# Optimization experiments

Measured on AMD Instinct MI355X. Metric: run time of the kernel, lower is better.

## Reference

```python
import jax, jax.numpy as jnp
import numpy as np

EMBED = 1024
HEADS = 16
HEAD_DIM = EMBED // HEADS
MLP = 4 * EMBED
EPS = 1e-6


def setup_inputs() -> dict:
    key = jax.random.key(0)
    ks = jax.random.split(key, 16)
    B, N, C = 2, 2048, EMBED
    x = jax.random.normal(ks[0], (B, N, C), dtype=jnp.float32)
    c = jax.random.normal(ks[1], (B, C), dtype=jnp.float32)
    attention_mask = jax.random.randint(ks[2], (B, N), 0, 2, dtype=jnp.int32)
    s = 0.02
    params = {
        "norm_w": jnp.ones((C,), jnp.float32),
        "scale_w": s * jax.random.normal(ks[3], (C, C), jnp.float32),
        "scale_b": s * jax.random.normal(ks[4], (C,), jnp.float32),
        "shift_w": s * jax.random.normal(ks[5], (C, C), jnp.float32),
        "shift_b": s * jax.random.normal(ks[6], (C,), jnp.float32),
        "qkv_w": s * jax.random.normal(ks[7], (3 * C, C), jnp.float32),
        "proj_w": s * jax.random.normal(ks[8], (C, C), jnp.float32),
        "proj_b": s * jax.random.normal(ks[9], (C,), jnp.float32),
        "mlp_w1": s * jax.random.normal(ks[10], (2 * MLP, C), jnp.float32),
        "mlp_b1": s * jax.random.normal(ks[11], (2 * MLP,), jnp.float32),
        "mlp_w2": s * jax.random.normal(ks[12], (C, MLP), jnp.float32),
        "mlp_b2": s * jax.random.normal(ks[13], (C,), jnp.float32),
    }
    return {"x": x, "c": c, "attention_mask": attention_mask, **params}


def _adaln(x, c, norm_w, scale_w, scale_b, shift_w, shift_b):
    sc = jax.nn.silu(c)
    shift = sc @ shift_w.T + shift_b                      # [B,C]
    scale = jnp.clip(sc @ scale_w.T + scale_b + 1.0, 0.1, 10.0)
    # RMSNorm: ||x|| * C^-0.5, clamped below by eps
    norm = jnp.maximum(jnp.linalg.norm(x, axis=-1, keepdims=True) * x.shape[-1] ** -0.5, EPS)
    h = x / norm * norm_w
    return h * scale[:, None, :] + shift[:, None, :]


def _attention(x, attention_mask, qkv_w, proj_w, proj_b):
    B, N, C = x.shape
    qkv = (x @ qkv_w.T).reshape(B, N, 3, HEADS, HEAD_DIM)
    q = qkv[:, :, 0].transpose(0, 2, 1, 3)  # [B,H,N,D]
    k = qkv[:, :, 1].transpose(0, 2, 1, 3)
    v = qkv[:, :, 2].transpose(0, 2, 1, 3)
    attn = jnp.einsum("bhnd,bhmd->bhnm", q, k) * (HEAD_DIM ** -0.5)
    mask = attention_mask[:, None, None, :]              # [B,1,1,N] over keys
    attn = jnp.where(mask == 0, -jnp.inf, attn)
    all_inf = jnp.all(attn == -jnp.inf, axis=-1, keepdims=True)
    attn = jnp.where(all_inf, 0.0, attn)
    p = jax.nn.softmax(attn, axis=-1)
    out = jnp.einsum("bhnm,bhmd->bhnd", p, v).transpose(0, 2, 1, 3).reshape(B, N, C)
    return out @ proj_w.T + proj_b


def _mlp(x, w1, b1, w2, b2):
    h = x @ w1.T + b1
    x1, x2 = jnp.split(h, 2, axis=-1)
    return (jax.nn.silu(x1) * x2) @ w2.T + b2


def reference(x, c, attention_mask, norm_w, scale_w, scale_b, shift_w, shift_b,
              qkv_w, proj_w, proj_b, mlp_w1, mlp_b1, mlp_w2, mlp_b2):
    x = x + _attention(_adaln(x, c, norm_w, scale_w, scale_b, shift_w, shift_b),
                       attention_mask, qkv_w, proj_w, proj_b)
    x = x + _mlp(_adaln(x, c, norm_w, scale_w, scale_b, shift_w, shift_b),
                 mlp_w1, mlp_b1, mlp_w2, mlp_b2)
    return x
```

## Files before the change

### kernel.cpp

```cpp
#include <hip/hip_runtime.h>
#include <cstdint>
#include <cstddef>

#define DEVINL __device__ __forceinline__

typedef __bf16 bf16x8 __attribute__((ext_vector_type(8)));
typedef float  f32x4  __attribute__((ext_vector_type(4)));


DEVINL unsigned short f2b(float f) {
  unsigned u = __builtin_bit_cast(unsigned, f);
  u += 0x7fffu + ((u >> 16) & 1u);
  return (unsigned short)(u >> 16);
}

DEVINL unsigned packtrunc(float a, float b) {
  unsigned ua = __builtin_bit_cast(unsigned, a);
  unsigned ub = __builtin_bit_cast(unsigned, b);
  return (ua >> 16) | (ub & 0xffff0000u);
}

DEVINL void async16(void* lds, const void* g) {
  __builtin_amdgcn_global_load_lds((const __attribute__((address_space(1))) unsigned*)g,
                                   (__attribute__((address_space(3))) unsigned*)lds,
                                   16, 0, 0);
}


__global__ void cvt4_kernel(const float* __restrict__ s0, const float* __restrict__ s1,
                            const float* __restrict__ s2, const float* __restrict__ s3,
                            unsigned short* __restrict__ d0, unsigned short* __restrict__ d1,
                            unsigned short* __restrict__ d2, unsigned short* __restrict__ d3) {
  int i = blockIdx.x * 256 + threadIdx.x;
  if (i < 786432) {
    float4 v = ((const float4*)s0)[i];
    ushort4 o; o.x = f2b(v.x); o.y = f2b(v.y); o.z = f2b(v.z); o.w = f2b(v.w);
    ((ushort4*)d0)[i] = o;
  } else if (i < 1048576) {
    int off = i - 786432;
    float4 v = ((const float4*)s1)[off];
    ushort4 o; o.x = f2b(v.x); o.y = f2b(v.y); o.z = f2b(v.z); o.w = f2b(v.w);
    ((ushort4*)d1)[off] = o;
  } else if (i < 3145728) {
    int off = i - 1048576;
    int row = off >> 8, col = off & 255;
    int rp = (row < 4096) ? (row << 1) : (((row - 4096) << 1) | 1);
    float4 v = ((const float4*)s2)[off];
    ushort4 o; o.x = f2b(v.x); o.y = f2b(v.y); o.z = f2b(v.z); o.w = f2b(v.w);
    ((ushort4*)d2)[rp * 256 + col] = o;
  } else {
    int off = i - 3145728;
    float4 v = ((const float4*)s3)[off];
    ushort4 o; o.x = f2b(v.x); o.y = f2b(v.y); o.z = f2b(v.z); o.w = f2b(v.w);
    ((ushort4*)d3)[off] = o;
  }
}


__global__ void cond_kernel(const float* __restrict__ c,
                            const float* __restrict__ scale_w, const float* __restrict__ scale_b,
                            const float* __restrict__ shift_w, const float* __restrict__ shift_b,
                            float* __restrict__ scale_o, float* __restrict__ shift_o) {
  __shared__ float sc[1024];
  __shared__ float red[2][4][64];
  int tid = threadIdx.x;
  int b = blockIdx.x >> 4, ch = blockIdx.x & 15;
  for (int i = tid; i < 1024; i += 256) {
    float cv = c[b * 1024 + i];
    sc[i] = cv / (1.f + __expf(-cv));
  }
  __syncthreads();
  int colidx = tid & 63, p = tid >> 6;
  int co = ch * 64 + colidx;
  float dsc = 0.f, dsh = 0.f;
  for (int i = 0; i < 256; ++i) {
    int kk = p * 256 + i;
    float s = sc[kk];
    dsc += s * scale_w[(size_t)co * 1024 + kk];
    dsh += s * shift_w[(size_t)co * 1024 + kk];
  }
  red[0][p][colidx] = dsc;
  red[1][p][colidx] = dsh;
  __syncthreads();
  if (p == 0) {
    float s4  = red[0][0][colidx] + red[0][1][colidx] + red[0][2][colidx] + red[0][3][colidx];
    float sh4 = red[1][0][colidx] + red[1][1][colidx] + red[1][2][colidx] + red[1][3][colidx];
    scale_o[b * 1024 + co] = fminf(fmaxf(s4 + scale_b[co] + 1.f, 0.1f), 10.f);
    shift_o[b * 1024 + co] = sh4 + shift_b[co];
  }
}


__global__ __launch_bounds__(256) void adaln_kernel(const float* __restrict__ x,
                                                    const float* __restrict__ norm_w,
                                                    const float* __restrict__ scale,
                                                    const float* __restrict__ shift,
                                                    unsigned short* __restrict__ h) {
  int row = blockIdx.x;
  int b = row >> 11;
  int tid = threadIdx.x;
  float4 v = ((const float4*)(x + (size_t)row * 1024))[tid];
  float ss = v.x * v.x + v.y * v.y + v.z * v.z + v.w * v.w;
  #pragma unroll
  for (int d = 32; d; d >>= 1) ss += __shfl_xor(ss, d);
  __shared__ float wsum[4];
  if ((tid & 63) == 0) wsum[tid >> 6] = ss;
  __syncthreads();
  float tot = wsum[0] + wsum[1] + wsum[2] + wsum[3];
  float inv = 1.f / fmaxf(sqrtf(tot * (1.f / 1024.f)), 1e-6f);
  float4 nw  = ((const float4*)norm_w)[tid];
  float4 scv = ((const float4*)(scale + b * 1024))[tid];
  float4 shv = ((const float4*)(shift + b * 1024))[tid];
  ushort4 o;
  o.x = f2b(v.x * inv * nw.x * scv.x + shv.x);
  o.y = f2b(v.y * inv * nw.y * scv.y + shv.y);
  o.z = f2b(v.z * inv * nw.z * scv.z + shv.z);
  o.w = f2b(v.w * inv * nw.w * scv.w + shv.w);
  ((ushort4*)(h + (size_t)row * 1024))[tid] = o;
}


template<int EPI, int MT>
__global__ __launch_bounds__(256, 1) void gemm_k(
    const unsigned short* __restrict__ A,
    const unsigned short* __restrict__ B0,
    const float* __restrict__ bias0,
    const float* __restrict__ resid,
    void* __restrict__ out0_, void* __restrict__ out1_, void* __restrict__ out2_,
    int M, int N, int K) {
  constexpr int MI = MT / 32;
  constexpr int A_SH = MT * 32;
  constexpr int COMPUTE_SH = 2 * A_SH + 2 * 4096;
  constexpr int STAGE_SH = (EPI == 1) ? 128 * 136 : (EPI == 2 ? 128 * 72 : 0);
  constexpr int SMEM_SH = (COMPUTE_SH > STAGE_SH) ? COMPUTE_SH : STAGE_SH;
  __shared__ __align__(16) unsigned short smem[SMEM_SH];
  unsigned short* As0 = smem;
  unsigned short* As1 = smem + A_SH;
  unsigned short* Bs0 = smem + 2 * A_SH;
  unsigned short* Bs1 = smem + 2 * A_SH + 4096;

  const int tid = threadIdx.x;
  const int wave = tid >> 6, lane = tid & 63;
  const int quad = lane >> 4, l16 = lane & 15;
  const int wm = (wave >> 1) * (MT / 2), wn = (wave & 1) * 64;
  const int bm = blockIdx.y * MT, bn = blockIdx.x * 128;

  f32x4 acc[MI][4] = {};

  const int steps = K >> 6;
  for (int s = 0; s < steps; ++s) {
    const int k0 = s << 6;
    __syncthreads();
    #pragma unroll
    for (int i = 0; i < MT / 64; ++i) {
      int cc = i * 256 + tid;
      int r = cc >> 2, ko = (cc & 3) << 3;
      size_t ga = (size_t)(bm + r) * K + k0 + ko;
      async16(As0 + (i * 2048 + wave * 512), A + ga);
      async16(As1 + (i * 2048 + wave * 512), A + ga + 32);
    }
    #pragma unroll
    for (int i = 0; i < 2; ++i) {
      int cc = i * 256 + tid;
      int r = cc >> 2, ko = (cc & 3) << 3;
      size_t gb = (size_t)(bn + r) * K + k0 + ko;
      async16(Bs0 + (i * 2048 + wave * 512), B0 + gb);
      async16(Bs1 + (i * 2048 + wave * 512), B0 + gb + 32);
    }
    __syncthreads();
    #pragma unroll
    for (int ks = 0; ks < 2; ++ks) {
      const unsigned short* Ah = ks ? As1 : As0;
      const unsigned short* Bh = ks ? Bs1 : Bs0;
      bf16x8 af[MI], bfr[4];
      #pragma unroll
      for (int mi = 0; mi < MI; ++mi)
        af[mi] = *reinterpret_cast<const bf16x8*>(&Ah[(wm + mi * 16 + l16) * 32 + quad * 8]);
      #pragma unroll
      for (int ni = 0; ni < 4; ++ni)
        bfr[ni] = *reinterpret_cast<const bf16x8*>(&Bh[(wn + ni * 16 + l16) * 32 + quad * 8]);
      #pragma unroll
      for (int mi = 0; mi < MI; ++mi)
        #pragma unroll
        for (int ni = 0; ni < 4; ++ni)
          acc[mi][ni] = __builtin_amdgcn_mfma_f32_16x16x32_bf16(af[mi], bfr[ni], acc[mi][ni], 0, 0, 0);
    }
  }

  if constexpr (EPI == 0) {
    #pragma unroll
    for (int mi = 0; mi < MI; ++mi) {
      #pragma unroll
      for (int ni = 0; ni < 4; ++ni) {
        int gc = bn + wn + ni * 16 + l16;
        #pragma unroll
        for (int r = 0; r < 4; ++r) {
          int gr = bm + wm + mi * 16 + quad * 4 + r;
          ((float*)out0_)[(size_t)gr * N + gc] = acc[mi][ni][r] + bias0[gc] + resid[(size_t)gr * N + gc];
        }
      }
    }
  } else if constexpr (EPI == 1) {
    const int region = bn >> 10;
    __syncthreads();
    #pragma unroll
    for (int mi = 0; mi < MI; ++mi) {
      #pragma unroll
      for (int ni = 0; ni < 4; ++ni) {
        int lc = wn + ni * 16 + l16;
        #pragma unroll
        for (int r = 0; r < 4; ++r) {
          int lr = wm + mi * 16 + quad * 4 + r;
          float v = acc[mi][ni][r];
          if (region == 0)      smem[lr * 136 + lc] = f2b(v * 0.125f);
          else if (region == 1) smem[lr * 136 + lc] = f2b(v);
          else                  smem[lc * 136 + lr] = f2b(v);
        }
      }
    }
    __syncthreads();
    const int b = bm >> 11;
    const int bnm = bn & 1023;
    if (region <= 1) {
      int lr = tid >> 1, hl = tid & 1;
      int n = (bm + lr) & 2047;
      int hh = (bnm >> 6) + hl;
      unsigned short* dst = (unsigned short*)(region == 0 ? out0_ : out1_) +
                            (((size_t)(b * 16 + hh)) * 2048 + n) * 64;
      const unsigned short* src = smem + lr * 136 + hl * 64;
      #pragma unroll
      for (int j = 0; j < 8; ++j)
        ((uint4*)dst)[j] = *(const uint4*)(src + j * 8);
    } else {
      int lc = tid >> 1, nh = tid & 1;
      int c2 = bnm + lc;
      int hh = c2 >> 6, d = c2 & 63;
      int nbase = (bm & 2047) + nh * 64;
      unsigned short* dst = (unsigned short*)out2_ +
                            (((size_t)(b * 16 + hh)) * 64 + d) * 2048 + nbase;
      const unsigned short* src = smem + lc * 136 + nh * 64;
      #pragma unroll
      for (int j = 0; j < 8; ++j)
        ((uint4*)dst)[j] = *(const uint4*)(src + j * 8);
    }
  } else {
    __syncthreads();
    #pragma unroll
    for (int mi = 0; mi < MI; ++mi) {
      #pragma unroll
      for (int ni = 0; ni < 4; ++ni) {
        int lc = wn + ni * 16 + l16;
        int gcp = bn + lc;
        int gi = gcp >> 1;
        float bias = bias0[(gcp & 1) ? 4096 + gi : gi];
        #pragma unroll
        for (int r = 0; r < 4; ++r) {
          int lr = wm + mi * 16 + quad * 4 + r;
          float v = acc[mi][ni][r] + bias;
          float p = __shfl_xor(v, 1);
          if ((l16 & 1) == 0) {
            float g = (v / (1.f + __expf(-v))) * p;
            smem[lr * 72 + (lc >> 1)] = f2b(g);
          }
        }
      }
    }
    __syncthreads();
    int lr = tid >> 1, ch = (tid & 1) * 32;
    unsigned short* dst = (unsigned short*)out0_ + (size_t)(bm + lr) * (N >> 1) + (bn >> 1) + ch;
    const unsigned short* src = smem + lr * 72 + ch;
    #pragma unroll
    for (int j = 0; j < 4; ++j)
      ((uint4*)dst)[j] = *(const uint4*)(src + j * 8);
  }
}


__global__ __launch_bounds__(512, 2) void gemm256_glu(
    const unsigned short* __restrict__ A,
    const unsigned short* __restrict__ B,
    const float* __restrict__ bias,
    unsigned short* __restrict__ out,
    int M, int N, int K) {
  __shared__ __align__(16) unsigned short smem[65536];

  const int tid  = threadIdx.x;
  const int wave = tid >> 6, lane = tid & 63;
  const int quad = lane >> 4, l16 = lane & 15;
  const int wm = (wave >> 2) * 128, wn = (wave & 3) * 64;

  const int lin = blockIdx.y * gridDim.x + blockIdx.x;
  const int xcd = lin & 7, idx = lin >> 3;
  const int bx = (xcd << 2) + (idx & 3);
  const int by = idx >> 2;
  const int bm = by * 256, bn = bx * 256;

  const int srow = tid >> 3;
  const int slc  = (tid & 7) ^ (srow & 7);
  const unsigned short* gA0 = A + (size_t)(bm + srow) * K + slc * 8;
  const unsigned short* gB0 = B + (size_t)(bn + srow) * K + slc * 8;
  const size_t rstep = (size_t)64 * K;

#define STAGE_A(h, tk, d) do { \
    const unsigned short* s_ = gA0 + (size_t)(h) * 128 * K + (size_t)(tk) * 64; \
    async16(smem + (d) * 16384 + (h) * 8192 + tid * 8, s_); \
    async16(smem + (d) * 16384 + (h) * 8192 + 4096 + tid * 8, s_ + rstep); \
  } while (0)
#define STAGE_B(h, tk, d) do { \
    const unsigned short* s_ = gB0 + (size_t)(h) * 128 * K + (size_t)(tk) * 64; \
    async16(smem + 32768 + (d) * 16384 + (h) * 8192 + tid * 8, s_); \
    async16(smem + 32768 + (d) * 16384 + (h) * 8192 + 4096 + tid * 8, s_ + rstep); \
  } while (0)

  const int pc0 = (quad ^ (l16 & 7)) * 8;
  const int pc1 = ((quad + 4) ^ (l16 & 7)) * 8;
  const int arow = wm + l16;
  const int brow = wn + l16;

  f32x4 acc[8][4] = {};
  bf16x8 bfr[4][2];
  const int T = K >> 6;
  const int JI = T >> 1;

  STAGE_B(0, 0, 0); STAGE_B(1, 0, 0);
  STAGE_A(0, 0, 0); STAGE_A(1, 0, 0);
  STAGE_B(0, 1, 1); STAGE_B(1, 1, 1);
  asm volatile("s_waitcnt vmcnt(4)" ::: "memory");
  __builtin_amdgcn_s_barrier();

#define READ_BFR(d) do { \
    _Pragma("unroll") \
    for (int ni = 0; ni < 4; ++ni) { \
      int rb = 32768 + (d) * 16384 + (brow + ni * 16) * 64; \
      bfr[ni][0] = *reinterpret_cast<const bf16x8*>(&smem[rb + pc0]); \
      bfr[ni][1] = *reinterpret_cast<const bf16x8*>(&smem[rb + pc1]); \
    } \
  } while (0)

#define PHASE(d, q, RB, STAGE_STMT, TAIL_STMT) do { \
    bf16x8 a00, a01, a10, a11; \
    if (RB) READ_BFR(d); \
    { int ra = (d) * 16384 + (arow + (2 * (q)) * 16) * 64; \
      a00 = *reinterpret_cast<const bf16x8*>(&smem[ra + pc0]); \
      a01 = *reinterpret_cast<const bf16x8*>(&smem[ra + pc1]); \
      a10 = *reinterpret_cast<const bf16x8*>(&smem[ra + 1024 + pc0]); \
      a11 = *reinterpret_cast<const bf16x8*>(&smem[ra + 1024 + pc1]); } \
    STAGE_STMT; \
    if (RB) asm volatile("s_waitcnt lgkmcnt(8)" ::: "memory"); \
    __builtin_amdgcn_s_barrier(); \
    asm volatile("s_waitcnt lgkmcnt(0)" ::: "memory"); \
    __builtin_amdgcn_sched_barrier(0); \
    __builtin_amdgcn_s_setprio(1); \
    _Pragma("unroll") \
    for (int ni = 0; ni < 4; ++ni) \
      acc[2 * (q)][ni] = __builtin_amdgcn_mfma_f32_16x16x32_bf16(a00, bfr[ni][0], acc[2 * (q)][ni], 0, 0, 0); \
    _Pragma("unroll") \
    for (int ni = 0; ni < 4; ++ni) \
      acc[2 * (q) + 1][ni] = __builtin_amdgcn_mfma_f32_16x16x32_bf16(a10, bfr[ni][0], acc[2 * (q) + 1][ni], 0, 0, 0); \
    _Pragma("unroll") \
    for (int ni = 0; ni < 4; ++ni) \
      acc[2 * (q)][ni] = __builtin_amdgcn_mfma_f32_16x16x32_bf16(a01, bfr[ni][1], acc[2 * (q)][ni], 0, 0, 0); \
    _Pragma("unroll") \
    for (int ni = 0; ni < 4; ++ni) \
      acc[2 * (q) + 1][ni] = __builtin_amdgcn_mfma_f32_16x16x32_bf16(a11, bfr[ni][1], acc[2 * (q) + 1][ni], 0, 0, 0); \
    __builtin_amdgcn_s_setprio(0); \
    TAIL_STMT; \
    __builtin_amdgcn_s_barrier(); \
  } while (0)

  for (int j = 0; j < JI; ++j) {
    const int t1 = 2 * j + 1, t2 = 2 * j + 2, t3 = 2 * j + 3;
    const bool g2 = (t2 < T), g3 = (t3 < T);
    PHASE(0, 0, 1, { STAGE_A(0, t1, 1); }, {});
    PHASE(0, 1, 0, { STAGE_A(1, t1, 1); }, {});
    PHASE(0, 2, 0, { if (g2) STAGE_B(0, t2, 0); }, {});
    PHASE(0, 3, 0, { if (g2) STAGE_B(1, t2, 0); },
          { if (g2) { asm volatile("s_waitcnt vmcnt(4)" ::: "memory"); }
            else    { asm volatile("s_waitcnt vmcnt(0)" ::: "memory"); } });
    PHASE(1, 0, 1, { if (g2) STAGE_A(0, t2, 0); }, {});
    PHASE(1, 1, 0, { if (g2) STAGE_A(1, t2, 0); }, {});
    PHASE(1, 2, 0, { if (g3) STAGE_B(0, t3, 1); }, {});
    PHASE(1, 3, 0, { if (g3) STAGE_B(1, t3, 1); },
          { if (j + 1 < JI) {
              if (g3) { asm volatile("s_waitcnt vmcnt(4)" ::: "memory"); }
              else    { asm volatile("s_waitcnt vmcnt(0)" ::: "memory"); } } });
  }

#undef PHASE
#undef READ_BFR
#undef STAGE_A
#undef STAGE_B

  #pragma unroll
  for (int ni = 0; ni < 4; ++ni) {
    int lc = wn + ni * 16 + l16;
    int gi = (bn + lc) >> 1;
    float bv = bias[(l16 & 1) ? 4096 + gi : gi];
    #pragma unroll
    for (int mi = 0; mi < 8; ++mi) {
      #pragma unroll
      for (int r = 0; r < 4; ++r) {
        float v = acc[mi][ni][r] + bv;
        float p = __shfl_xor(v, 1);
        if ((l16 & 1) == 0) {
          int lr = wm + mi * 16 + quad * 4 + r;
          float g = (v / (1.f + __expf(-v))) * p;
          smem[lr * 136 + (lc >> 1)] = f2b(g);
        }
      }
    }
  }
  __syncthreads();
  {
    int lr = tid >> 1, half = (tid & 1) * 64;
    unsigned short* dst = out + (size_t)(bm + lr) * (N >> 1) + (bn >> 1) + half;
    const unsigned short* src = smem + lr * 136 + half;
    #pragma unroll
    for (int j = 0; j < 8; ++j)
      ((uint4*)dst)[j] = *(const uint4*)(src + j * 8);
  }
}


__global__ __launch_bounds__(512, 1) void attn_kernel(
    const unsigned short* __restrict__ q, const unsigned short* __restrict__ k,
    const unsigned short* __restrict__ vt, const int* __restrict__ amask,
    unsigned short* __restrict__ o) {
  const int bh = blockIdx.x;
  const int b = bh >> 4, h = bh & 15;
  const int qt = blockIdx.y;
  const int tid = threadIdx.x;
  const int wave = tid >> 6, lane = tid & 63;
  const int quad = lane >> 4, l16 = lane & 15;
  const int h7 = l16 & 7;
  const int kc0 = (quad ^ h7) * 8;
  const int kc1 = ((quad + 4) ^ h7) * 8;

  const unsigned short* qb = q  + (size_t)bh * 2048 * 64;
  const unsigned short* kb = k  + (size_t)bh * 2048 * 64;
  const unsigned short* vb = vt + (size_t)bh * 64 * 2048;

  __shared__ __align__(16) unsigned short Ks[2][64 * 64];
  __shared__ __align__(16) unsigned short Vs[2][64 * 64];
  __shared__ __align__(16) unsigned short Ps[8 * 16 * 72];
  __shared__ float biasf[2][64];

  unsigned short* PsW = Ps + wave * 1152;

  const int qrow = qt * 128 + wave * 16 + l16;
  bf16x8 qa0 = *reinterpret_cast<const bf16x8*>(&qb[(size_t)qrow * 64 + quad * 8]);
  bf16x8 qa1 = *reinterpret_cast<const bf16x8*>(&qb[(size_t)qrow * 64 + 32 + quad * 8]);

  f32x4 oacc[4] = {};
  float mrow = -30000.f, lrow = 0.f;

  uint4 kpre, vpre;
  {
    int key = tid >> 3, dl = (tid & 7) ^ (key & 7);
    kpre = *(const uint4*)(kb + key * 64 + dl * 8);
    int d = tid >> 3, kl = (tid & 7) ^ (d & 7);
    vpre = *(const uint4*)(vb + (size_t)d * 2048 + kl * 8);
  }
  int mv = (tid < 64) ? amask[b * 2048 + tid] : 0;

  for (int kt = 0; kt < 32; ++kt) {
    const int cb = kt & 1;
    ((uint4*)Ks[cb])[tid] = kpre;
    ((uint4*)Vs[cb])[tid] = vpre;
    if (tid < 64) biasf[cb][tid] = mv ? 0.f : -30000.f;
    __syncthreads();

    if (kt + 1 < 32) {
      int key = tid >> 3, dl = (tid & 7) ^ (key & 7);
      kpre = *(const uint4*)(kb + (size_t)(kt + 1) * 4096 + key * 64 + dl * 8);
      int d = tid >> 3, kl = (tid & 7) ^ (d & 7);
      vpre = *(const uint4*)(vb + (size_t)d * 2048 + (kt + 1) * 64 + kl * 8);
      mv = (tid < 64) ? amask[b * 2048 + (kt + 1) * 64 + tid] : 0;
    }

    f32x4 st[4];
    __builtin_amdgcn_s_setprio(1);
    #pragma unroll
    for (int nt = 0; nt < 4; ++nt) {
      bf16x8 ka0 = *reinterpret_cast<const bf16x8*>(&Ks[cb][(nt * 16 + l16) * 64 + kc0]);
      bf16x8 ka1 = *reinterpret_cast<const bf16x8*>(&Ks[cb][(nt * 16 + l16) * 64 + kc1]);
      f32x4 bv = *reinterpret_cast<const f32x4*>(&biasf[cb][nt * 16 + quad * 4]);
      f32x4 z = {};
      z = __builtin_amdgcn_mfma_f32_16x16x32_bf16(ka0, qa0, z, 0, 0, 0);
      z = __builtin_amdgcn_mfma_f32_16x16x32_bf16(ka1, qa1, z, 0, 0, 0);
      st[nt] = z + bv;
    }
    __builtin_amdgcn_s_setprio(0);

    float m01 = fmaxf(fmaxf(st[0][0], st[0][1]), fmaxf(st[0][2], st[0][3]));
    float m23 = fmaxf(fmaxf(st[1][0], st[1][1]), fmaxf(st[1][2], st[1][3]));
    float m45 = fmaxf(fmaxf(st[2][0], st[2][1]), fmaxf(st[2][2], st[2][3]));
    float m67 = fmaxf(fmaxf(st[3][0], st[3][1]), fmaxf(st[3][2], st[3][3]));
    float tm = fmaxf(fmaxf(m01, m23), fmaxf(m45, m67));
    tm = fmaxf(tm, __shfl_xor(tm, 16));
    tm = fmaxf(tm, __shfl_xor(tm, 32));

    const bool defer = __all(tm <= mrow + 8.f);
    if (!defer) {
      float mnew = fmaxf(mrow, tm);
      float alpha = __expf(mrow - mnew);
      mrow = mnew;
      float a0 = __shfl(alpha, quad * 4 + 0);
      float a1 = __shfl(alpha, quad * 4 + 1);
      float a2 = __shfl(alpha, quad * 4 + 2);
      float a3 = __shfl(alpha, quad * 4 + 3);
      #pragma unroll
      for (int dt = 0; dt < 4; ++dt) {
        oacc[dt][0] *= a0; oacc[dt][1] *= a1; oacc[dt][2] *= a2; oacc[dt][3] *= a3;
      }
      lrow *= alpha;
    }

    float rs = 0.f;
    #pragma unroll
    for (int nt = 0; nt < 4; ++nt) {
      float p0 = __expf(st[nt][0] - mrow);
      float p1 = __expf(st[nt][1] - mrow);
      float p2 = __expf(st[nt][2] - mrow);
      float p3 = __expf(st[nt][3] - mrow);
      rs += (p0 + p1) + (p2 + p3);
      uint2 w;
      w.x = packtrunc(p0, p1);
      w.y = packtrunc(p2, p3);
      *(uint2*)&PsW[l16 * 72 + nt * 16 + quad * 4] = w;
    }
    rs += __shfl_xor(rs, 16);
    rs += __shfl_xor(rs, 32);
    lrow += rs;

    bf16x8 pa0 = *reinterpret_cast<const bf16x8*>(&PsW[l16 * 72 + quad * 8]);
    bf16x8 pa1 = *reinterpret_cast<const bf16x8*>(&PsW[l16 * 72 + 32 + quad * 8]);
    __builtin_amdgcn_s_setprio(1);
    #pragma unroll
    for (int dt = 0; dt < 4; ++dt) {
      bf16x8 vb0 = *reinterpret_cast<const bf16x8*>(&Vs[cb][(dt * 16 + l16) * 64 + kc0]);
      bf16x8 vb1 = *reinterpret_cast<const bf16x8*>(&Vs[cb][(dt * 16 + l16) * 64 + kc1]);
      oacc[dt] = __builtin_amdgcn_mfma_f32_16x16x32_bf16(pa0, vb0, oacc[dt], 0, 0, 0);
      oacc[dt] = __builtin_amdgcn_mfma_f32_16x16x32_bf16(pa1, vb1, oacc[dt], 0, 0, 0);
    }
    __builtin_amdgcn_s_setprio(0);
  }

  float invl = lrow > 0.f ? 1.f / lrow : 0.f;
  float i0 = __shfl(invl, quad * 4 + 0);
  float i1 = __shfl(invl, quad * 4 + 1);
  float i2 = __shfl(invl, quad * 4 + 2);
  float i3 = __shfl(invl, quad * 4 + 3);
  __syncthreads();
  #pragma unroll
  for (int dt = 0; dt < 4; ++dt) {
    int lr = wave * 16 + quad * 4;
    Ps[(lr + 0) * 72 + dt * 16 + l16] = f2b(oacc[dt][0] * i0);
    Ps[(lr + 1) * 72 + dt * 16 + l16] = f2b(oacc[dt][1] * i1);
    Ps[(lr + 2) * 72 + dt * 16 + l16] = f2b(oacc[dt][2] * i2);
    Ps[(lr + 3) * 72 + dt * 16 + l16] = f2b(oacc[dt][3] * i3);
  }
  __syncthreads();
  {
    int lr = tid >> 2, cb2 = (tid & 3) * 16;
    int n = qt * 128 + lr;
    unsigned short* dst = o + ((size_t)(b * 2048 + n)) * 1024 + h * 64 + cb2;
    const unsigned short* src = Ps + lr * 72 + cb2;
    ((uint4*)dst)[0] = *(const uint4*)(src);
    ((uint4*)dst)[1] = *(const uint4*)(src + 8);
  }
}


extern "C" void kernel_launch(void* const* d_in, const int* in_sizes, int n_in,
                              void* d_out, int out_size, void* d_ws, size_t ws_size,
                              hipStream_t stream) {
  const float* x       = (const float*)d_in[0];
  const float* c       = (const float*)d_in[1];
  const int*   amask   = (const int*)d_in[2];
  const float* norm_w  = (const float*)d_in[3];
  const float* scale_w = (const float*)d_in[4];
  const float* scale_b = (const float*)d_in[5];
  const float* shift_w = (const float*)d_in[6];
  const float* shift_b = (const float*)d_in[7];
  const float* qkv_w   = (const float*)d_in[8];
  const float* proj_w  = (const float*)d_in[9];
  const float* proj_b  = (const float*)d_in[10];
  const float* mlp_w1  = (const float*)d_in[11];
  const float* mlp_b1  = (const float*)d_in[12];
  const float* mlp_w2  = (const float*)d_in[13];
  const float* mlp_b2  = (const float*)d_in[14];

  char* ws = (char*)d_ws;
  unsigned short* wqkv  = (unsigned short*)(ws + 0);
  unsigned short* wproj = (unsigned short*)(ws + 6291456);
  unsigned short* wmlp1 = (unsigned short*)(ws + 8388608);
  unsigned short* wmlp2 = (unsigned short*)(ws + 25165824);
  float* scale_o        = (float*)(ws + 33554432);
  float* shift_o        = (float*)(ws + 33562624);
  unsigned short* hbuf  = (unsigned short*)(ws + 33570816);
  unsigned short* qbuf  = (unsigned short*)(ws + 41959424);
  unsigned short* kbuf  = (unsigned short*)(ws + 50348032);
  unsigned short* vbuf  = (unsigned short*)(ws + 58736640);
  unsigned short* abuf  = (unsigned short*)(ws + 67125248);
  unsigned short* gbuf  = qbuf;
  float* x1             = (float*)(ws + 75513856);

  cvt4_kernel<<<16384, 256, 0, stream>>>(qkv_w, proj_w, mlp_w1, mlp_w2,
                                         wqkv, wproj, wmlp1, wmlp2);

  cond_kernel<<<32, 256, 0, stream>>>(c, scale_w, scale_b, shift_w, shift_b, scale_o, shift_o);

  adaln_kernel<<<4096, 256, 0, stream>>>(x, norm_w, scale_o, shift_o, hbuf);

  gemm_k<1, 128><<<dim3(24, 32), 256, 0, stream>>>(hbuf, wqkv, nullptr, nullptr,
                                                   qbuf, kbuf, vbuf, 4096, 3072, 1024);

  attn_kernel<<<dim3(32, 16), 512, 0, stream>>>(qbuf, kbuf, vbuf, amask, abuf);

  gemm_k<0, 64><<<dim3(8, 64), 256, 0, stream>>>(abuf, wproj, proj_b, x,
                                                 x1, nullptr, nullptr, 4096, 1024, 1024);

  adaln_kernel<<<4096, 256, 0, stream>>>(x1, norm_w, scale_o, shift_o, hbuf);

  gemm256_glu<<<dim3(32, 16), 512, 0, stream>>>(hbuf, wmlp1, mlp_b1, gbuf, 4096, 8192, 1024);

  gemm_k<0, 64><<<dim3(8, 64), 256, 0, stream>>>(gbuf, wmlp2, mlp_b2, x1,
                                                 d_out, nullptr, nullptr, 4096, 1024, 4096);

  (void)in_sizes; (void)n_in; (void)out_size; (void)ws_size;
}
```

Before: 468.4 us.

## Double-buffer GEMM LDS stages to overlap global loads with MFMA compute

```diff
diff --git a/kernel.cpp b/kernel.cpp
--- a/kernel.cpp
+++ b/kernel.cpp
@@ -130,14 +130,11 @@
     int M, int N, int K) {
   constexpr int MI = MT / 32;
   constexpr int A_SH = MT * 32;
-  constexpr int COMPUTE_SH = 2 * A_SH + 2 * 4096;
+  constexpr int SLOT_SH = 2 * A_SH + 2 * 4096;
+  constexpr int RING_SH = 2 * SLOT_SH;
   constexpr int STAGE_SH = (EPI == 1) ? 128 * 136 : (EPI == 2 ? 128 * 72 : 0);
-  constexpr int SMEM_SH = (COMPUTE_SH > STAGE_SH) ? COMPUTE_SH : STAGE_SH;
+  constexpr int SMEM_SH = (RING_SH > STAGE_SH) ? RING_SH : STAGE_SH;
   __shared__ __align__(16) unsigned short smem[SMEM_SH];
-  unsigned short* As0 = smem;
-  unsigned short* As1 = smem + A_SH;
-  unsigned short* Bs0 = smem + 2 * A_SH;
-  unsigned short* Bs1 = smem + 2 * A_SH + 4096;
 
   const int tid = threadIdx.x;
   const int wave = tid >> 6, lane = tid & 63;
@@ -146,32 +143,46 @@
   const int bm = blockIdx.y * MT, bn = blockIdx.x * 128;
 
   f32x4 acc[MI][4] = {};
-
   const int steps = K >> 6;
-  for (int s = 0; s < steps; ++s) {
+
+  auto STAGE = [&](int s, int r) {
     const int k0 = s << 6;
-    __syncthreads();
+    unsigned short* base = smem + r * SLOT_SH;
     #pragma unroll
     for (int i = 0; i < MT / 64; ++i) {
       int cc = i * 256 + tid;
-      int r = cc >> 2, ko = (cc & 3) << 3;
-      size_t ga = (size_t)(bm + r) * K + k0 + ko;
-      async16(As0 + (i * 2048 + wave * 512), A + ga);
-      async16(As1 + (i * 2048 + wave * 512), A + ga + 32);
+      int rr = cc >> 2, ko = (cc & 3) << 3;
+      size_t ga = (size_t)(bm + rr) * K + k0 + ko;
+      async16(base + (i * 2048 + wave * 512), A + ga);
+      async16(base + A_SH + (i * 2048 + wave * 512), A + ga + 32);
     }
     #pragma unroll
     for (int i = 0; i < 2; ++i) {
       int cc = i * 256 + tid;
-      int r = cc >> 2, ko = (cc & 3) << 3;
-      size_t gb = (size_t)(bn + r) * K + k0 + ko;
-      async16(Bs0 + (i * 2048 + wave * 512), B0 + gb);
-      async16(Bs1 + (i * 2048 + wave * 512), B0 + gb + 32);
-    }
-    __syncthreads();
+      int rr = cc >> 2, ko = (cc & 3) << 3;
+      size_t gb = (size_t)(bn + rr) * K + k0 + ko;
+      async16(base + 2 * A_SH + (i * 2048 + wave * 512), B0 + gb);
+      async16(base + 2 * A_SH + 4096 + (i * 2048 + wave * 512), B0 + gb + 32);
+    }
+  };
+
+  STAGE(0, 0);
+  if (steps > 1) STAGE(1, 1);
+
+  for (int s = 0; s < steps; ++s) {
+    if (s < steps - 1) {
+      if constexpr (MT == 64) asm volatile("s_waitcnt vmcnt(6)" ::: "memory");
+      else                    asm volatile("s_waitcnt vmcnt(8)" ::: "memory");
+    } else {
+      asm volatile("s_waitcnt vmcnt(0)" ::: "memory");
+    }
+    __builtin_amdgcn_s_barrier();
+
+    const unsigned short* base = smem + (s & 1) * SLOT_SH;
     #pragma unroll
     for (int ks = 0; ks < 2; ++ks) {
-      const unsigned short* Ah = ks ? As1 : As0;
-      const unsigned short* Bh = ks ? Bs1 : Bs0;
+      const unsigned short* Ah = base + (ks ? A_SH : 0);
+      const unsigned short* Bh = base + 2 * A_SH + (ks ? 4096 : 0);
       bf16x8 af[MI], bfr[4];
       #pragma unroll
       for (int mi = 0; mi < MI; ++mi)
@@ -185,6 +196,10 @@
         for (int ni = 0; ni < 4; ++ni)
           acc[mi][ni] = __builtin_amdgcn_mfma_f32_16x16x32_bf16(af[mi], bfr[ni], acc[mi][ni], 0, 0, 0);
     }
+
+    asm volatile("s_waitcnt lgkmcnt(0)" ::: "memory");
+    __builtin_amdgcn_s_barrier();
+    if (s + 2 < steps) STAGE(s + 2, s & 1);
   }
 
   if constexpr (EPI == 0) {
```

Measured after the change: 456.9 us. 1.03x faster.
